# Kernel tuning notes

Hardware: AMD Instinct MI355X
Metric: run time of the kernel (lower is better)

The kernel has to match this reference:

```python
import jax, jax.numpy as jnp
import numpy as np
import math

Q_SHAPES = [(20, 30), (10, 15), (5, 8)]
S_SHAPES = [(20, 30), (10, 15), (5, 8)]
C_IN = 256
C_OUT = 256
NUM_HEADS = 8


def _rel_indices(q_shapes, s_shapes):
    # Faithful translation of QSGA.get_rel_indices: block matrix over pyramid levels.
    rows = []
    for hq, wq in q_shapes:
        cols = []
        for hs, ws in s_shapes:
            ind = np.arange(ws)[None, :] / ws - np.arange(hq)[:, None] / hq  # [hq, ws]
            sc = math.sqrt(ws * hq)
            indx = np.tile(ind, (wq, hs)) * sc                              # [hq*wq, hs*ws]
            indy = np.repeat(np.repeat(ind, wq, axis=0), hs, axis=1) * sc   # [hq*wq, hs*ws]
            indd = indx ** 2 + indy ** 2
            cols.append(np.stack([indd, indx, indy], axis=-1))
        rows.append(np.concatenate(cols, axis=1))
    return jnp.asarray(np.concatenate(rows, axis=0)[None].astype(np.float32))  # [1, Nq, Ns, 3]


def setup_inputs() -> dict:
    key = jax.random.key(0)
    ks = jax.random.split(key, 8)
    B, M = 2, 5
    Nq = sum(h * w for h, w in Q_SHAPES)
    Ns = sum(h * w for h, w in S_SHAPES)
    std = 0.02
    # local_init: v = identity, pos_proj weight zero except col0 = -alphas, gating = ones
    min_a, max_a = 0.002, 0.2
    alphas = np.array([min_a + (max_a - min_a) / NUM_HEADS ** 2.5 * i ** 2.5 for i in range(NUM_HEADS)], np.float32)
    Wp = np.zeros((NUM_HEADS, 3), np.float32)
    Wp[:, 0] = -alphas
    return {
        "q_feat": jax.random.normal(ks[0], (B, Nq, C_IN), jnp.float32),
        "s_feat": jax.random.normal(ks[1], (M, Ns, C_IN), jnp.float32),
        "rel_indices": _rel_indices(Q_SHAPES, S_SHAPES),
        "Wq": jax.random.normal(ks[2], (C_OUT, C_IN), jnp.float32) * std,
        "bq": jnp.zeros((C_OUT,), jnp.float32),
        "Wk": jax.random.normal(ks[3], (C_OUT, C_IN), jnp.float32) * std,
        "bk": jnp.zeros((C_OUT,), jnp.float32),
        "Wv": jnp.eye(C_OUT, C_IN, dtype=jnp.float32),
        "bv": jnp.zeros((C_OUT,), jnp.float32),
        "Wp": jnp.asarray(Wp),
        "bp": jnp.zeros((NUM_HEADS,), jnp.float32),
        "Wo": jax.random.normal(ks[4], (C_OUT, C_OUT), jnp.float32) * std,
        "bo": jnp.zeros((C_OUT,), jnp.float32),
        "gating": jnp.ones((NUM_HEADS,), jnp.float32),
    }


def reference(q_feat, s_feat, rel_indices, Wq, bq, Wk, bk, Wv, bv, Wp, bp, Wo, bo, gating):
    B, Nq, _ = q_feat.shape
    M, Ns, _ = s_feat.shape
    H = gating.shape[0]
    C = Wq.shape[0]
    Dh = C // H
    scale = Dh ** -0.5
    # projections -> [B,H,Nq,Dh], [M,H,Ns,Dh]
    q = (q_feat @ Wq.T + bq).reshape(B, Nq, H, Dh).transpose(0, 2, 1, 3)
    k = (s_feat @ Wk.T + bk).reshape(M, Ns, H, Dh).transpose(0, 2, 1, 3)
    # content scores over all (query image, support image) pairs: [B,M,H,Nq,Ns]
    patch = jnp.einsum('bhqd,mhsd->bmhqs', q, k) * scale
    patch = jax.nn.softmax(patch, axis=-1)
    # positional scores: [1,Nq,Ns,3] -> [1,H,Nq,Ns]
    pos = jax.nn.softmax((rel_indices @ Wp.T + bp).transpose(0, 3, 1, 2), axis=-1)
    g = jax.nn.sigmoid(gating)[None, None, :, None, None]  # [1,1,H,1,1]
    attn = (1.0 - g) * patch + g * pos[:, None]            # broadcast pos over B,M
    attn = attn / attn.sum(axis=-1, keepdims=True)
    v = (s_feat @ Wv.T + bv).reshape(M, Ns, H, Dh).transpose(0, 2, 1, 3)  # [M,H,Ns,Dh]
    out = jnp.einsum('bmhqs,mhsd->bmhqd', attn, v)          # [B,M,H,Nq,Dh]
    out = out.transpose(0, 1, 3, 2, 4).reshape(B, M, Nq, C)  # [B,M,Nq,C]
    return out @ Wo.T + bo
```

## Files before the change

kernel.cpp:

```cpp
#include <hip/hip_runtime.h>
#include <hip/hip_bf16.h>
#include <math.h>

#define B_ 2
#define M_ 5
#define H_ 8
#define C_ 256
#define DH 32
#define NQ 790
#define NS 790
#define QT32 25
#define VROW 800
#define PPAD 800

typedef __attribute__((ext_vector_type(8))) __bf16 bf16x8;
typedef __attribute__((ext_vector_type(16))) float f32x16;
typedef unsigned int u32;
typedef unsigned short u16;

#define LOG2E 1.4426950408889634f

static __device__ __forceinline__ u16 bf16bits(float v) {
  union { __bf16 h; u16 u; } x; x.h = (__bf16)v; return x.u;
}
static __device__ __forceinline__ u32 pack2bf(float a, float b) {
  union { __bf16 h[2]; u32 u; } x; x.h[0] = (__bf16)a; x.h[1] = (__bf16)b; return x.u;
}

#define POS_N 395
#define GEMM0 395
#define PADBLK 544
#define WCVT0 545

#define PROJ_STEP(ACC, BY)                                                 \
  {                                                                        \
    int bcol_ = (BY) * 64 + wc * 32 + lo;                                  \
    const float* wf_ = Wm + (size_t)bcol_ * C_ + k0;                       \
    float4 g0_ = *(const float4*)wf_, g1_ = *(const float4*)(wf_ + 4);     \
    bf16x8 b_;                                                             \
    b_[0]=(__bf16)g0_.x; b_[1]=(__bf16)g0_.y; b_[2]=(__bf16)g0_.z; b_[3]=(__bf16)g0_.w; \
    b_[4]=(__bf16)g1_.x; b_[5]=(__bf16)g1_.y; b_[6]=(__bf16)g1_.z; b_[7]=(__bf16)g1_.w; \
    ACC = __builtin_amdgcn_mfma_f32_32x32x16_bf16(a_, b_, ACC, 0, 0, 0);   \
  }

#define STORE_QK(ACC, BY)                                                  \
  {                                                                        \
    int bcol_ = (BY) * 64 + wc * 32 + lo;                                  \
    float bvv_ = bias[bcol_];                                              \
    _Pragma("unroll")                                                      \
    for (int r_ = 0; r_ < 16; ++r_) {                                      \
      int row_ = (r_ & 3) + 8 * (r_ >> 2) + 4 * hi;                        \
      int grow_ = grow0 + wr * 32 + row_;                                  \
      if (grow_ < R) {                                                     \
        float v_ = (ACC[r_] + bvv_) * scale;                               \
        int seg_ = grow_ / 790, srow_ = grow_ - seg_ * 790;                \
        size_t addr_ = ((size_t)(seg_ * H_ + (bcol_ >> 5)) * 790 + srow_) * 32 + (bcol_ & 31); \
        outp[addr_] = bf16bits(v_);                                        \
      }                                                                    \
    }                                                                      \
  }

#define STORE_V(ACC, BY)                                                   \
  {                                                                        \
    int bcol_ = (BY) * 64 + wc * 32 + lo;                                  \
    float bvv_ = bias[bcol_];                                              \
    int cIn_ = wc * 32 + lo;                                               \
    _Pragma("unroll")                                                      \
    for (int r_ = 0; r_ < 16; ++r_) {                                      \
      int row_ = (r_ & 3) + 8 * (r_ >> 2) + 4 * hi;                        \
      Tls[cIn_][wr * 32 + row_] = bf16bits(ACC[r_] + bvv_);                \
    }                                                                      \
    __syncthreads();                                                       \
    {                                                                      \
      int c_l = tid >> 2, g_l = (tid & 3) * 16;                            \
      int gcol = (BY) * 64 + c_l;                                          \
      int g0v = grow0 + g_l;                                               \
      u16 vals_[16];                                                       \
      _Pragma("unroll")                                                    \
      for (int i_ = 0; i_ < 16; ++i_) vals_[i_] = Tls[c_l][g_l + i_];      \
      int mA_ = g0v / 790, mB_ = (g0v + 15) / 790;                         \
      u16* dst_ = vT2 + (size_t)gcol * (M_ * VROW);                        \
      if (mB_ < M_ && mA_ == mB_) {                                        \
        size_t base_ = (size_t)mA_ * VROW + (g0v - mA_ * 790);             \
        *(uint4*)(dst_ + base_)     = *(uint4*)(vals_);                    \
        *(uint4*)(dst_ + base_ + 8) = *(uint4*)(vals_ + 8);                \
      } else {                                                             \
        _Pragma("unroll")                                                  \
        for (int i_ = 0; i_ < 16; ++i_) {                                  \
          int g_ = g0v + i_;                                               \
          if (g_ < M_ * 790) {                                             \
            int mm_ = g_ / 790, ss_ = g_ - mm_ * 790;                      \
            dst_[(size_t)mm_ * VROW + ss_] = vals_[i_];                    \
          }                                                                \
        }                                                                  \
      }                                                                    \
    }                                                                      \
    __syncthreads();                                                       \
  }

__global__ __launch_bounds__(256) void stage1(const float* __restrict__ qf,
    const float* __restrict__ sf, const float* __restrict__ rel,
    const float* __restrict__ Wq, const float* __restrict__ bq,
    const float* __restrict__ Wk, const float* __restrict__ bk,
    const float* __restrict__ Wv, const float* __restrict__ bv,
    const float* __restrict__ Wp, const float* __restrict__ bp,
    const float* __restrict__ Wo,
    u16* __restrict__ qb, u16* __restrict__ kb, u16* __restrict__ vT2,
    u16* __restrict__ pp, u16* __restrict__ wob, float qscale) {
  __shared__ u16 Tls[64][72];
  int bid = blockIdx.x;
  int tid = threadIdx.x;

  if (bid < POS_N) {
    int wave = tid >> 6, lane = tid & 63;
    int q = bid * 2 + (wave >> 1);
    int h0 = (wave & 1) * 4;
    float rd[13], rx[13], ry[13];
#pragma unroll
    for (int t = 0; t < 13; ++t) {
      int s = lane + 64 * t;
      if (s < NS) {
        const float* rp = rel + ((size_t)q * NS + s) * 3;
        rd[t] = rp[0]; rx[t] = rp[1]; ry[t] = rp[2];
      } else { rd[t] = 0.f; rx[t] = 0.f; ry[t] = 0.f; }
    }
    for (int h = h0; h < h0 + 4; ++h) {
      float w0 = Wp[h * 3] * LOG2E, w1 = Wp[h * 3 + 1] * LOG2E,
            w2 = Wp[h * 3 + 2] * LOG2E, b = bp[h] * LOG2E;
      float lg[13], sm = 0.f;
#pragma unroll
      for (int t = 0; t < 13; ++t) {
        int s = lane + 64 * t;
        float v = rd[t] * w0 + rx[t] * w1 + ry[t] * w2 + b;
        lg[t] = exp2f((s < NS) ? v : -1e30f);
        sm += lg[t];
      }
#pragma unroll
      for (int off = 32; off; off >>= 1) sm += __shfl_xor(sm, off);
      float inv = 1.f / sm;
#pragma unroll
      for (int t = 0; t < 13; ++t) {
        int s = lane + 64 * t;
        if (s < PPAD)
          pp[((size_t)h * NQ + q) * PPAD + s] = (s < NS) ? bf16bits(lg[t] * inv) : (u16)0;
      }
    }
    return;
  }

  if (bid == PADBLK) {
    int c = tid;
#pragma unroll
    for (int m = 0; m < M_; ++m) {
      u32* p = (u32*)(vT2 + (size_t)c * (M_ * VROW) + m * VROW + 790);
#pragma unroll
      for (int i = 0; i < 5; ++i) p[i] = 0;
    }
    return;
  }

  if (bid >= WCVT0) {
    int base = (bid - WCVT0) * 8192;
#pragma unroll
    for (int k = 0; k < 4; ++k) {
      int idx = base + k * 2048 + tid * 8;
      const float* src = Wo + idx;
      float4 f0 = *(const float4*)src, f1 = *(const float4*)(src + 4);
      u16 v[8];
      v[0]=bf16bits(f0.x); v[1]=bf16bits(f0.y); v[2]=bf16bits(f0.z); v[3]=bf16bits(f0.w);
      v[4]=bf16bits(f1.x); v[5]=bf16bits(f1.y); v[6]=bf16bits(f1.z); v[7]=bf16bits(f1.w);
      *(uint4*)(wob + idx) = *(uint4*)v;
    }
    return;
  }

  int j = bid - GEMM0;
  const float* A; const float* Wm; const float* bias; int R; float scale; int role; int bx;
  if (j < 25)      { A = qf; Wm = Wq; bias = bq; R = B_ * NQ; scale = qscale; role = 0; bx = j; }
  else if (j < 87) { A = sf; Wm = Wk; bias = bk; R = M_ * NS; scale = 1.f;    role = 1; bx = j - 25; }
  else             { A = sf; Wm = Wv; bias = bv; R = M_ * NS; scale = 1.f;    role = 2; bx = j - 87; }

  int wave = tid >> 6, lane = tid & 63;
  int lo = lane & 31, hi = lane >> 5;
  int wr = wave >> 1, wc = wave & 1;
  int grow0 = bx * 64;
  int arow = grow0 + wr * 32 + lo;
  int ar = arow < R ? arow : R - 1;

  f32x16 acc0, acc1, acc2, acc3;
#pragma unroll
  for (int r = 0; r < 16; ++r) { acc0[r] = 0.f; acc1[r] = 0.f; acc2[r] = 0.f; acc3[r] = 0.f; }
#pragma unroll
  for (int kk = 0; kk < 16; ++kk) {
    int k0 = kk * 16 + hi * 8;
    const float* af = A + (size_t)ar * C_ + k0;
    float4 f0 = *(const float4*)af, f1 = *(const float4*)(af + 4);
    bf16x8 a_;
    a_[0]=(__bf16)f0.x; a_[1]=(__bf16)f0.y; a_[2]=(__bf16)f0.z; a_[3]=(__bf16)f0.w;
    a_[4]=(__bf16)f1.x; a_[5]=(__bf16)f1.y; a_[6]=(__bf16)f1.z; a_[7]=(__bf16)f1.w;
    PROJ_STEP(acc0, 0);
    PROJ_STEP(acc1, 1);
    PROJ_STEP(acc2, 2);
    PROJ_STEP(acc3, 3);
  }

  if (role < 2) {
    u16* outp = (role == 0) ? qb : kb;
    STORE_QK(acc0, 0);
    STORE_QK(acc1, 1);
    STORE_QK(acc2, 2);
    STORE_QK(acc3, 3);
  } else {
    STORE_V(acc0, 0);
    STORE_V(acc1, 1);
    STORE_V(acc2, 2);
    STORE_V(acc3, 3);
  }
}

static __device__ __forceinline__ void wave_range(int wave, int& st, int& en) {
  st = wave * 6 + (wave ? 1 : 0);
  en = st + (wave ? 6 : 7);
}

#define SM_PV(c_, OACC, ZR, FV0, FV1)                                      \
  {                                                                        \
    float p_[16];                                                          \
    _Pragma("unroll")                                                      \
    for (int r_ = 0; r_ < 16; ++r_) p_[r_] = exp2f(c_[r_]);                \
    float s0_ = p_[0]+p_[1],  s1_ = p_[2]+p_[3];                           \
    float s2_ = p_[4]+p_[5],  s3_ = p_[6]+p_[7];                           \
    float s4_ = p_[8]+p_[9],  s5_ = p_[10]+p_[11];                         \
    float s6_ = p_[12]+p_[13], s7_ = p_[14]+p_[15];                        \
    s0_ += s1_; s2_ += s3_; s4_ += s5_; s6_ += s7_;                        \
    s0_ += s2_; s4_ += s6_;                                                \
    float ts_ = s0_ + s4_;                                                 \
    { float xa_ = ts_, xb_ = ts_;                                          \
      asm("v_permlane32_swap_b32 %0, %1" : "+v"(xa_), "+v"(xb_));          \
      ZR += xa_ + xb_; }                                                   \
    u32 pk_[8];                                                            \
    _Pragma("unroll")                                                      \
    for (int t_ = 0; t_ < 8; ++t_) pk_[t_] = pack2bf(p_[2*t_], p_[2*t_+1]); \
    asm("v_permlane32_swap_b32 %0, %1" : "+v"(pk_[0]), "+v"(pk_[2]));      \
    asm("v_permlane32_swap_b32 %0, %1" : "+v"(pk_[1]), "+v"(pk_[3]));      \
    asm("v_permlane32_swap_b32 %0, %1" : "+v"(pk_[4]), "+v"(pk_[6]));      \
    asm("v_permlane32_swap_b32 %0, %1" : "+v"(pk_[5]), "+v"(pk_[7]));      \
    union { u32 u[4]; bf16x8 v; } pa_, pb_;                                \
    pa_.u[0] = pk_[0]; pa_.u[1] = pk_[1]; pa_.u[2] = pk_[2]; pa_.u[3] = pk_[3]; \
    pb_.u[0] = pk_[4]; pb_.u[1] = pk_[5]; pb_.u[2] = pk_[6]; pb_.u[3] = pk_[7]; \
    OACC = __builtin_amdgcn_mfma_f32_32x32x16_bf16(FV0, pa_.v, OACC, 0, 0, 0); \
    OACC = __builtin_amdgcn_mfma_f32_32x32x16_bf16(FV1, pb_.v, OACC, 0, 0, 0); \
  }

#define TILE_BODY(KC0,KC1, KN0,KN1, IT, NT)                                \
  {                                                                        \
     \
    bf16x8 vf0 = *(const bf16x8*)(vbase + (IT) * 32 + hi8);                \
    bf16x8 vf1 = *(const bf16x8*)(vbase + (IT) * 32 + 16 + hi8);           \
    bf16x8 pf0 = *(const bf16x8*)(pbase + (IT) * 32 + hi8);                \
    bf16x8 pf1 = *(const bf16x8*)(pbase + (IT) * 32 + 16 + hi8);           \
                                             \
    int srn_ = (NT) * 32 + lo; if (srn_ >= NS) srn_ = NS - 1;              \
    KN0 = *(const bf16x8*)(kbase + (size_t)srn_ * 32 + hi8);               \
    KN1 = *(const bf16x8*)(kbase + (size_t)srn_ * 32 + 16 + hi8);          \
    f32x16 c0_ = kZero, c1_ = kZero;                                       \
    c0_ = __builtin_amdgcn_mfma_f32_32x32x16_bf16(KC0, fq00, c0_, 0, 0, 0);\
    c0_ = __builtin_amdgcn_mfma_f32_32x32x16_bf16(KC1, fq01, c0_, 0, 0, 0);\
    c1_ = __builtin_amdgcn_mfma_f32_32x32x16_bf16(KC0, fq10, c1_, 0, 0, 0);\
    c1_ = __builtin_amdgcn_mfma_f32_32x32x16_bf16(KC1, fq11, c1_, 0, 0, 0);\
    Opos = __builtin_amdgcn_mfma_f32_32x32x16_bf16(vf0, pf0, Opos, 0, 0, 0);\
    Opos = __builtin_amdgcn_mfma_f32_32x32x16_bf16(vf1, pf1, Opos, 0, 0, 0);\
    if ((IT) == 24) {                                                      \
      _Pragma("unroll")                                                    \
      for (int r_ = 0; r_ < 16; ++r_) {                                    \
        int sl_ = (r_ & 3) + 8 * (r_ >> 2) + 4 * hi;                       \
        if (768 + sl_ >= NS) { c0_[r_] = -1e30f; c1_[r_] = -1e30f; }       \
      }                                                                    \
    }                                                                      \
    SM_PV(c0_, O0, Z0, vf0, vf1);                                          \
    SM_PV(c1_, O1, Z1, vf0, vf1);                                          \
  }

__global__ __launch_bounds__(256, 3) void attn2(const u16* __restrict__ qb,
    const u16* __restrict__ kb, const u16* __restrict__ vT2,
    const u16* __restrict__ pp, const float* __restrict__ gating,
    u16* __restrict__ opb) {
  int logical = (blockIdx.x & 7) * 125 + (blockIdx.x >> 3);
  int m  = logical % M_;
  int r2 = logical / M_;
  int qt = r2 % QT32;
  int h  = r2 / QT32;
  int tid = threadIdx.x;
  int wave = tid >> 6, lane = tid & 63;
  int lo = lane & 31, hi = lane >> 5, hi8 = hi * 8;
  int qg = qt * 32 + lo;
  int qc = qg < NQ ? qg : NQ - 1;

  const u16* qp0 = qb + ((size_t)(0 * H_ + h) * NQ + qc) * 32 + hi8;
  const u16* qp1 = qb + ((size_t)(1 * H_ + h) * NQ + qc) * 32 + hi8;
  bf16x8 fq00 = *(const bf16x8*)qp0;
  bf16x8 fq01 = *(const bf16x8*)(qp0 + 16);
  bf16x8 fq10 = *(const bf16x8*)qp1;
  bf16x8 fq11 = *(const bf16x8*)(qp1 + 16);
  const u16* kbase = kb + ((size_t)(m * H_ + h) * NS) * 32;
  const u16* vbase = vT2 + (size_t)(h * DH + lo) * (M_ * VROW) + m * VROW;
  const u16* pbase = pp + ((size_t)h * NQ + qc) * PPAD;

  f32x16 O0, O1, Opos, kZero;
#pragma unroll
  for (int r = 0; r < 16; ++r) { O0[r] = 0.f; O1[r] = 0.f; Opos[r] = 0.f; kZero[r] = 0.f; }
  float Z0 = 0.f, Z1 = 0.f;
  int st, en; wave_range(wave, st, en);

  bf16x8 ak0, ak1, bk0, bk1;
  {
    int sr0 = st * 32 + lo; if (sr0 >= NS) sr0 = NS - 1;
    ak0 = *(const bf16x8*)(kbase + (size_t)sr0 * 32 + hi8);
    ak1 = *(const bf16x8*)(kbase + (size_t)sr0 * 32 + 16 + hi8);
  }
  int it = st;
  while (it + 2 <= en) {
    TILE_BODY(ak0, ak1, bk0, bk1, it, it + 1);
    int nt2 = (it + 2 < en) ? it + 2 : it + 1;
    TILE_BODY(bk0, bk1, ak0, ak1, it + 1, nt2);
    it += 2;
  }
  if (it < en) TILE_BODY(ak0, ak1, bk0, bk1, it, it);

  __shared__ float Os[4][32][33];
  __shared__ float Zs[4][32];
  float g = 1.f / (1.f + __expf(-gating[h]));
  int d = tid & 31, qi = tid >> 5;
  float oc0[4], oc1[4];

#pragma unroll
  for (int r = 0; r < 16; ++r) {
    int dd = (r & 3) + 8 * (r >> 2) + 4 * hi;
    Os[wave][dd][lo] = O0[r];
  }
  if (hi == 0) Zs[wave][lo] = Z0;
  __syncthreads();
#pragma unroll
  for (int k = 0; k < 4; ++k) {
    int ql = qi + 8 * k;
    float zg = Zs[0][ql] + Zs[1][ql] + Zs[2][ql] + Zs[3][ql];
    float oc = Os[0][d][ql] + Os[1][d][ql] + Os[2][d][ql] + Os[3][d][ql];
    oc0[k] = (1.f - g) * oc / zg;
  }
  __syncthreads();

#pragma unroll
  for (int r = 0; r < 16; ++r) {
    int dd = (r & 3) + 8 * (r >> 2) + 4 * hi;
    Os[wave][dd][lo] = O1[r];
  }
  if (hi == 0) Zs[wave][lo] = Z1;
  __syncthreads();
#pragma unroll
  for (int k = 0; k < 4; ++k) {
    int ql = qi + 8 * k;
    float zg = Zs[0][ql] + Zs[1][ql] + Zs[2][ql] + Zs[3][ql];
    float oc = Os[0][d][ql] + Os[1][d][ql] + Os[2][d][ql] + Os[3][d][ql];
    oc1[k] = (1.f - g) * oc / zg;
  }
  __syncthreads();

#pragma unroll
  for (int r = 0; r < 16; ++r) {
    int dd = (r & 3) + 8 * (r >> 2) + 4 * hi;
    Os[wave][dd][lo] = Opos[r];
  }
  __syncthreads();
  u16* out0 = opb + ((size_t)(0 * M_ + m) * NQ) * C_ + h * DH + d;
  u16* out1 = opb + ((size_t)(1 * M_ + m) * NQ) * C_ + h * DH + d;
#pragma unroll
  for (int k = 0; k < 4; ++k) {
    int ql = qi + 8 * k;
    int qgl = qt * 32 + ql;
    if (qgl < NQ) {
      float op = Os[0][d][ql] + Os[1][d][ql] + Os[2][d][ql] + Os[3][d][ql];
      out0[(size_t)qgl * C_] = bf16bits(oc0[k] + g * op);
      out1[(size_t)qgl * C_] = bf16bits(oc1[k] + g * op);
    }
  }
}

__global__ __launch_bounds__(256) void out_gemm(const u16* __restrict__ Ap,
    const u16* __restrict__ Wb, const float* __restrict__ bias,
    float* __restrict__ outp, int R) {
  int tid = threadIdx.x;
  int wave = tid >> 6, lane = tid & 63;
  int lo = lane & 31, hi = lane >> 5;
  int wr = wave >> 1, wc = wave & 1;
  int arow = blockIdx.x * 64 + wr * 32 + lo;
  int ar = arow < R ? arow : R - 1;
  int bcolA = blockIdx.y * 128 + wc * 32 + lo;
  int bcolB = bcolA + 64;
  f32x16 accA, accB;
#pragma unroll
  for (int r = 0; r < 16; ++r) { accA[r] = 0.f; accB[r] = 0.f; }
#pragma unroll
  for (int kk = 0; kk < 16; ++kk) {
    int k0 = kk * 16 + hi * 8;
    bf16x8 a = *(const bf16x8*)(Ap + (size_t)ar * C_ + k0);
    bf16x8 bA = *(const bf16x8*)(Wb + (size_t)bcolA * C_ + k0);
    bf16x8 bB = *(const bf16x8*)(Wb + (size_t)bcolB * C_ + k0);
    accA = __builtin_amdgcn_mfma_f32_32x32x16_bf16(a, bA, accA, 0, 0, 0);
    accB = __builtin_amdgcn_mfma_f32_32x32x16_bf16(a, bB, accB, 0, 0, 0);
  }
  float bvA = bias[bcolA], bvB = bias[bcolB];
#pragma unroll
  for (int r = 0; r < 16; ++r) {
    int row = (r & 3) + 8 * (r >> 2) + 4 * hi;
    int grow = blockIdx.x * 64 + wr * 32 + row;
    if (grow < R) {
      outp[(size_t)grow * C_ + bcolA] = accA[r] + bvA;
      outp[(size_t)grow * C_ + bcolB] = accB[r] + bvB;
    }
  }
}

extern "C" void kernel_launch(void* const* d_in, const int* in_sizes, int n_in,
                              void* d_out, int out_size, void* d_ws, size_t ws_size,
                              hipStream_t stream) {
  const float* q_feat = (const float*)d_in[0];
  const float* s_feat = (const float*)d_in[1];
  const float* rel    = (const float*)d_in[2];
  const float* Wq = (const float*)d_in[3];
  const float* bq = (const float*)d_in[4];
  const float* Wk = (const float*)d_in[5];
  const float* bk = (const float*)d_in[6];
  const float* Wv = (const float*)d_in[7];
  const float* bv = (const float*)d_in[8];
  const float* Wp = (const float*)d_in[9];
  const float* bp = (const float*)d_in[10];
  const float* Wo = (const float*)d_in[11];
  const float* bo = (const float*)d_in[12];
  const float* gating = (const float*)d_in[13];
  float* out = (float*)d_out;

  char* w = (char*)d_ws;
  u16* qb  = (u16*)w;
  u16* kb  = (u16*)(w + 808960);
  u16* vT2 = (u16*)(w + 2831360);
  u16* pp  = (u16*)(w + 4879360);
  u16* opb = (u16*)(w + 14991360);
  u16* wob = (u16*)(w + 19036160);

  const float QSCALE = 0.17677669529663687f * 1.4426950408889634f;

  stage1<<<553, 256, 0, stream>>>(q_feat, s_feat, rel, Wq, bq, Wk, bk, Wv, bv,
                                  Wp, bp, Wo, qb, kb, vT2, pp, wob, QSCALE);
  attn2<<<1000, 256, 0, stream>>>(qb, kb, vT2, pp, gating, opb);
  out_gemm<<<dim3(124, 2), 256, 0, stream>>>(opb, wob, bo, out, B_ * M_ * NQ);
}
```

Before: 69.90 us.

## Process two query tiles per attention block to reuse K/V fragment loads

Each attention block now handles a pair of 32-row query tiles (A and B), so every K and V fragment loaded per key tile feeds twice as many MFMAs. The grid shrinks from 1000 to 520 blocks and launch bounds drop to 2 blocks per CU to make room for the doubled accumulators. Inline-asm permlane swaps are also replaced with the compiler builtin, which may let the compiler schedule them better. The cost is higher register pressure, lower occupancy, one extra padded tile of wasted work (13 pairs for 25 tiles), and a longer serialized epilogue with more barriers.

```diff
diff --git a/kernel.cpp b/kernel.cpp
--- a/kernel.cpp
+++ b/kernel.cpp
@@ -10,11 +10,13 @@
 #define NQ 790
 #define NS 790
 #define QT32 25
+#define QTP 13
 #define VROW 800
 #define PPAD 800
 
 typedef __attribute__((ext_vector_type(8))) __bf16 bf16x8;
 typedef __attribute__((ext_vector_type(16))) float f32x16;
+typedef __attribute__((ext_vector_type(2))) unsigned int u32x2;
 typedef unsigned int u32;
 typedef unsigned short u16;
 
@@ -25,6 +27,16 @@
 }
 static __device__ __forceinline__ u32 pack2bf(float a, float b) {
   union { __bf16 h[2]; u32 u; } x; x.h[0] = (__bf16)a; x.h[1] = (__bf16)b; return x.u;
+}
+static __device__ __forceinline__ float halfswap_sum(float ts) {
+  union { float f; u32 u; } c; c.f = ts;
+  u32x2 r = __builtin_amdgcn_permlane32_swap(c.u, c.u, false, false);
+  union { u32 u; float f; } a, b; a.u = r[0]; b.u = r[1];
+  return a.f + b.f;
+}
+static __device__ __forceinline__ void pswap(u32& x, u32& y) {
+  u32x2 r = __builtin_amdgcn_permlane32_swap(x, y, false, false);
+  x = r[0]; y = r[1];
 }
 
 #define POS_N 395
@@ -234,17 +246,14 @@
     float s6_ = p_[12]+p_[13], s7_ = p_[14]+p_[15];                        \
     s0_ += s1_; s2_ += s3_; s4_ += s5_; s6_ += s7_;                        \
     s0_ += s2_; s4_ += s6_;                                                \
-    float ts_ = s0_ + s4_;                                                 \
-    { float xa_ = ts_, xb_ = ts_;                                          \
-      asm("v_permlane32_swap_b32 %0, %1" : "+v"(xa_), "+v"(xb_));          \
-      ZR += xa_ + xb_; }                                                   \
+    ZR += halfswap_sum(s0_ + s4_);                                         \
     u32 pk_[8];                                                            \
     _Pragma("unroll")                                                      \
     for (int t_ = 0; t_ < 8; ++t_) pk_[t_] = pack2bf(p_[2*t_], p_[2*t_+1]); \
-    asm("v_permlane32_swap_b32 %0, %1" : "+v"(pk_[0]), "+v"(pk_[2]));      \
-    asm("v_permlane32_swap_b32 %0, %1" : "+v"(pk_[1]), "+v"(pk_[3]));      \
-    asm("v_permlane32_swap_b32 %0, %1" : "+v"(pk_[4]), "+v"(pk_[6]));      \
-    asm("v_permlane32_swap_b32 %0, %1" : "+v"(pk_[5]), "+v"(pk_[7]));      \
+    pswap(pk_[0], pk_[2]);                                                 \
+    pswap(pk_[1], pk_[3]);                                                 \
+    pswap(pk_[4], pk_[6]);                                                 \
+    pswap(pk_[5], pk_[7]);                                                 \
     union { u32 u[4]; bf16x8 v; } pa_, pb_;                                \
     pa_.u[0] = pk_[0]; pa_.u[1] = pk_[1]; pa_.u[2] = pk_[2]; pa_.u[3] = pk_[3]; \
     pb_.u[0] = pk_[4]; pb_.u[1] = pk_[5]; pb_.u[2] = pk_[6]; pb_.u[3] = pk_[7]; \
@@ -252,64 +261,90 @@
     OACC = __builtin_amdgcn_mfma_f32_32x32x16_bf16(FV1, pb_.v, OACC, 0, 0, 0); \
   }
 
+#define MASK_TAIL(c_)                                                      \
+    { _Pragma("unroll")                                                    \
+      for (int r_ = 0; r_ < 16; ++r_) {                                    \
+        int sl_ = (r_ & 3) + 8 * (r_ >> 2) + 4 * hi;                       \
+        if (768 + sl_ >= NS) c_[r_] = -1e30f;                              \
+      } }
+
 #define TILE_BODY(KC0,KC1, KN0,KN1, IT, NT)                                \
   {                                                                        \
-     \
     bf16x8 vf0 = *(const bf16x8*)(vbase + (IT) * 32 + hi8);                \
     bf16x8 vf1 = *(const bf16x8*)(vbase + (IT) * 32 + 16 + hi8);           \
-    bf16x8 pf0 = *(const bf16x8*)(pbase + (IT) * 32 + hi8);                \
-    bf16x8 pf1 = *(const bf16x8*)(pbase + (IT) * 32 + 16 + hi8);           \
-                                             \
+    bf16x8 pA0 = *(const bf16x8*)(pbA + (IT) * 32 + hi8);                  \
+    bf16x8 pA1 = *(const bf16x8*)(pbA + (IT) * 32 + 16 + hi8);             \
+    bf16x8 pB0 = *(const bf16x8*)(pbB + (IT) * 32 + hi8);                  \
+    bf16x8 pB1 = *(const bf16x8*)(pbB + (IT) * 32 + 16 + hi8);             \
     int srn_ = (NT) * 32 + lo; if (srn_ >= NS) srn_ = NS - 1;              \
     KN0 = *(const bf16x8*)(kbase + (size_t)srn_ * 32 + hi8);               \
     KN1 = *(const bf16x8*)(kbase + (size_t)srn_ * 32 + 16 + hi8);          \
-    f32x16 c0_ = kZero, c1_ = kZero;                                       \
-    c0_ = __builtin_amdgcn_mfma_f32_32x32x16_bf16(KC0, fq00, c0_, 0, 0, 0);\
-    c0_ = __builtin_amdgcn_mfma_f32_32x32x16_bf16(KC1, fq01, c0_, 0, 0, 0);\
-    c1_ = __builtin_amdgcn_mfma_f32_32x32x16_bf16(KC0, fq10, c1_, 0, 0, 0);\
-    c1_ = __builtin_amdgcn_mfma_f32_32x32x16_bf16(KC1, fq11, c1_, 0, 0, 0);\
-    Opos = __builtin_amdgcn_mfma_f32_32x32x16_bf16(vf0, pf0, Opos, 0, 0, 0);\
-    Opos = __builtin_amdgcn_mfma_f32_32x32x16_bf16(vf1, pf1, Opos, 0, 0, 0);\
-    if ((IT) == 24) {                                                      \
-      _Pragma("unroll")                                                    \
-      for (int r_ = 0; r_ < 16; ++r_) {                                    \
-        int sl_ = (r_ & 3) + 8 * (r_ >> 2) + 4 * hi;                       \
-        if (768 + sl_ >= NS) { c0_[r_] = -1e30f; c1_[r_] = -1e30f; }       \
-      }                                                                    \
-    }                                                                      \
-    SM_PV(c0_, O0, Z0, vf0, vf1);                                          \
-    SM_PV(c1_, O1, Z1, vf0, vf1);                                          \
-  }
-
-__global__ __launch_bounds__(256, 3) void attn2(const u16* __restrict__ qb,
+    OposA = __builtin_amdgcn_mfma_f32_32x32x16_bf16(vf0, pA0, OposA, 0, 0, 0); \
+    OposA = __builtin_amdgcn_mfma_f32_32x32x16_bf16(vf1, pA1, OposA, 0, 0, 0); \
+    OposB = __builtin_amdgcn_mfma_f32_32x32x16_bf16(vf0, pB0, OposB, 0, 0, 0); \
+    OposB = __builtin_amdgcn_mfma_f32_32x32x16_bf16(vf1, pB1, OposB, 0, 0, 0); \
+    {                                                                      \
+      f32x16 c0_ = kZero, c1_ = kZero;                                     \
+      c0_ = __builtin_amdgcn_mfma_f32_32x32x16_bf16(KC0, fqA00, c0_, 0, 0, 0); \
+      c0_ = __builtin_amdgcn_mfma_f32_32x32x16_bf16(KC1, fqA01, c0_, 0, 0, 0); \
+      c1_ = __builtin_amdgcn_mfma_f32_32x32x16_bf16(KC0, fqA10, c1_, 0, 0, 0); \
+      c1_ = __builtin_amdgcn_mfma_f32_32x32x16_bf16(KC1, fqA11, c1_, 0, 0, 0); \
+      if ((IT) == 24) { MASK_TAIL(c0_); MASK_TAIL(c1_); }                  \
+      SM_PV(c0_, OA0, ZA0, vf0, vf1);                                      \
+      SM_PV(c1_, OA1, ZA1, vf0, vf1);                                      \
+    }                                                                      \
+    {                                                                      \
+      f32x16 c0_ = kZero, c1_ = kZero;                                     \
+      c0_ = __builtin_amdgcn_mfma_f32_32x32x16_bf16(KC0, fqB00, c0_, 0, 0, 0); \
+      c0_ = __builtin_amdgcn_mfma_f32_32x32x16_bf16(KC1, fqB01, c0_, 0, 0, 0); \
+      c1_ = __builtin_amdgcn_mfma_f32_32x32x16_bf16(KC0, fqB10, c1_, 0, 0, 0); \
+      c1_ = __builtin_amdgcn_mfma_f32_32x32x16_bf16(KC1, fqB11, c1_, 0, 0, 0); \
+      if ((IT) == 24) { MASK_TAIL(c0_); MASK_TAIL(c1_); }                  \
+      SM_PV(c0_, OB0, ZB0, vf0, vf1);                                      \
+      SM_PV(c1_, OB1, ZB1, vf0, vf1);                                      \
+    }                                                                      \
+  }
+
+__global__ __launch_bounds__(256, 2) void attn2(const u16* __restrict__ qb,
     const u16* __restrict__ kb, const u16* __restrict__ vT2,
     const u16* __restrict__ pp, const float* __restrict__ gating,
     u16* __restrict__ opb) {
-  int logical = (blockIdx.x & 7) * 125 + (blockIdx.x >> 3);
-  int m  = logical % M_;
-  int r2 = logical / M_;
-  int qt = r2 % QT32;
-  int h  = r2 / QT32;
+  int logical = (blockIdx.x & 7) * 65 + (blockIdx.x >> 3);
+  int m   = logical % M_;
+  int r2  = logical / M_;
+  int qtp = r2 % QTP;
+  int h   = r2 / QTP;
+  int qtA = qtp * 2, qtB = qtp * 2 + 1;
   int tid = threadIdx.x;
   int wave = tid >> 6, lane = tid & 63;
   int lo = lane & 31, hi = lane >> 5, hi8 = hi * 8;
-  int qg = qt * 32 + lo;
-  int qc = qg < NQ ? qg : NQ - 1;
-
-  const u16* qp0 = qb + ((size_t)(0 * H_ + h) * NQ + qc) * 32 + hi8;
-  const u16* qp1 = qb + ((size_t)(1 * H_ + h) * NQ + qc) * 32 + hi8;
-  bf16x8 fq00 = *(const bf16x8*)qp0;
-  bf16x8 fq01 = *(const bf16x8*)(qp0 + 16);
-  bf16x8 fq10 = *(const bf16x8*)qp1;
-  bf16x8 fq11 = *(const bf16x8*)(qp1 + 16);
+  int qgA = qtA * 32 + lo;  int qcA = qgA < NQ ? qgA : NQ - 1;
+  int qgB = qtB * 32 + lo;  int qcB = qgB < NQ ? qgB : NQ - 1;
+
+  const u16* qpA0 = qb + ((size_t)(0 * H_ + h) * NQ + qcA) * 32 + hi8;
+  const u16* qpA1 = qb + ((size_t)(1 * H_ + h) * NQ + qcA) * 32 + hi8;
+  const u16* qpB0 = qb + ((size_t)(0 * H_ + h) * NQ + qcB) * 32 + hi8;
+  const u16* qpB1 = qb + ((size_t)(1 * H_ + h) * NQ + qcB) * 32 + hi8;
+  bf16x8 fqA00 = *(const bf16x8*)qpA0;
+  bf16x8 fqA01 = *(const bf16x8*)(qpA0 + 16);
+  bf16x8 fqA10 = *(const bf16x8*)qpA1;
+  bf16x8 fqA11 = *(const bf16x8*)(qpA1 + 16);
+  bf16x8 fqB00 = *(const bf16x8*)qpB0;
+  bf16x8 fqB01 = *(const bf16x8*)(qpB0 + 16);
+  bf16x8 fqB10 = *(const bf16x8*)qpB1;
+  bf16x8 fqB11 = *(const bf16x8*)(qpB1 + 16);
   const u16* kbase = kb + ((size_t)(m * H_ + h) * NS) * 32;
   const u16* vbase = vT2 + (size_t)(h * DH + lo) * (M_ * VROW) + m * VROW;
-  const u16* pbase = pp + ((size_t)h * NQ + qc) * PPAD;
-
-  f32x16 O0, O1, Opos, kZero;
-#pragma unroll
-  for (int r = 0; r < 16; ++r) { O0[r] = 0.f; O1[r] = 0.f; Opos[r] = 0.f; kZero[r] = 0.f; }
-  float Z0 = 0.f, Z1 = 0.f;
+  const u16* pbA = pp + ((size_t)h * NQ + qcA) * PPAD;
+  const u16* pbB = pp + ((size_t)h * NQ + qcB) * PPAD;
+
+  f32x16 OA0, OA1, OB0, OB1, OposA, OposB, kZero;
+#pragma unroll
+  for (int r = 0; r < 16; ++r) {
+    OA0[r] = 0.f; OA1[r] = 0.f; OB0[r] = 0.f; OB1[r] = 0.f;
+    OposA[r] = 0.f; OposB[r] = 0.f; kZero[r] = 0.f;
+  }
+  float ZA0 = 0.f, ZA1 = 0.f, ZB0 = 0.f, ZB1 = 0.f;
   int st, en; wave_range(wave, st, en);
 
   bf16x8 ak0, ak1, bk0, bk1;
@@ -331,58 +366,64 @@
   __shared__ float Zs[4][32];
   float g = 1.f / (1.f + __expf(-gating[h]));
   int d = tid & 31, qi = tid >> 5;
-  float oc0[4], oc1[4];
-
-#pragma unroll
-  for (int r = 0; r < 16; ++r) {
-    int dd = (r & 3) + 8 * (r >> 2) + 4 * hi;
-    Os[wave][dd][lo] = O0[r];
-  }
-  if (hi == 0) Zs[wave][lo] = Z0;
-  __syncthreads();
-#pragma unroll
-  for (int k = 0; k < 4; ++k) {
-    int ql = qi + 8 * k;
-    float zg = Zs[0][ql] + Zs[1][ql] + Zs[2][ql] + Zs[3][ql];
-    float oc = Os[0][d][ql] + Os[1][d][ql] + Os[2][d][ql] + Os[3][d][ql];
-    oc0[k] = (1.f - g) * oc / zg;
-  }
-  __syncthreads();
-
-#pragma unroll
-  for (int r = 0; r < 16; ++r) {
-    int dd = (r & 3) + 8 * (r >> 2) + 4 * hi;
-    Os[wave][dd][lo] = O1[r];
-  }
-  if (hi == 0) Zs[wave][lo] = Z1;
-  __syncthreads();
-#pragma unroll
-  for (int k = 0; k < 4; ++k) {
-    int ql = qi + 8 * k;
-    float zg = Zs[0][ql] + Zs[1][ql] + Zs[2][ql] + Zs[3][ql];
-    float oc = Os[0][d][ql] + Os[1][d][ql] + Os[2][d][ql] + Os[3][d][ql];
-    oc1[k] = (1.f - g) * oc / zg;
-  }
-  __syncthreads();
-
-#pragma unroll
-  for (int r = 0; r < 16; ++r) {
-    int dd = (r & 3) + 8 * (r >> 2) + 4 * hi;
-    Os[wave][dd][lo] = Opos[r];
-  }
-  __syncthreads();
-  u16* out0 = opb + ((size_t)(0 * M_ + m) * NQ) * C_ + h * DH + d;
-  u16* out1 = opb + ((size_t)(1 * M_ + m) * NQ) * C_ + h * DH + d;
-#pragma unroll
-  for (int k = 0; k < 4; ++k) {
-    int ql = qi + 8 * k;
-    int qgl = qt * 32 + ql;
-    if (qgl < NQ) {
-      float op = Os[0][d][ql] + Os[1][d][ql] + Os[2][d][ql] + Os[3][d][ql];
-      out0[(size_t)qgl * C_] = bf16bits(oc0[k] + g * op);
-      out1[(size_t)qgl * C_] = bf16bits(oc1[k] + g * op);
-    }
-  }
+
+#define MERGE_QT(OX0, OX1, OPOSX, ZX0, ZX1, QT)                            \
+  {                                                                        \
+    float oc0[4], oc1[4];                                                  \
+    _Pragma("unroll")                                                      \
+    for (int r = 0; r < 16; ++r) {                                         \
+      int dd = (r & 3) + 8 * (r >> 2) + 4 * hi;                            \
+      Os[wave][dd][lo] = OX0[r];                                           \
+    }                                                                      \
+    if (hi == 0) Zs[wave][lo] = ZX0;                                       \
+    __syncthreads();                                                       \
+    _Pragma("unroll")                                                      \
+    for (int k = 0; k < 4; ++k) {                                          \
+      int ql = qi + 8 * k;                                                 \
+      float zg = Zs[0][ql] + Zs[1][ql] + Zs[2][ql] + Zs[3][ql];            \
+      float oc = Os[0][d][ql] + Os[1][d][ql] + Os[2][d][ql] + Os[3][d][ql];\
+      oc0[k] = (1.f - g) * oc / zg;                                        \
+    }                                                                      \
+    __syncthreads();                                                       \
+    _Pragma("unroll")                                                      \
+    for (int r = 0; r < 16; ++r) {                                         \
+      int dd = (r & 3) + 8 * (r >> 2) + 4 * hi;                            \
+      Os[wave][dd][lo] = OX1[r];                                           \
+    }                                                                      \
+    if (hi == 0) Zs[wave][lo] = ZX1;                                       \
+    __syncthreads();                                                       \
+    _Pragma("unroll")                                                      \
+    for (int k = 0; k < 4; ++k) {                                          \
+      int ql = qi + 8 * k;                                                 \
+      float zg = Zs[0][ql] + Zs[1][ql] + Zs[2][ql] + Zs[3][ql];            \
+      float oc = Os[0][d][ql] + Os[1][d][ql] + Os[2][d][ql] + Os[3][d][ql];\
+      oc1[k] = (1.f - g) * oc / zg;                                        \
+    }                                                                      \
+    __syncthreads();                                                       \
+    _Pragma("unroll")                                                      \
+    for (int r = 0; r < 16; ++r) {                                         \
+      int dd = (r & 3) + 8 * (r >> 2) + 4 * hi;                            \
+      Os[wave][dd][lo] = OPOSX[r];                                         \
+    }                                                                      \
+    __syncthreads();                                                       \
+    u16* out0 = opb + ((size_t)(0 * M_ + m) * NQ) * C_ + h * DH + d;       \
+    u16* out1 = opb + ((size_t)(1 * M_ + m) * NQ) * C_ + h * DH + d;       \
+    _Pragma("unroll")                                                      \
+    for (int k = 0; k < 4; ++k) {                                          \
+      int ql = qi + 8 * k;                                                 \
+      int qgl = (QT) * 32 + ql;                                            \
+      if (qgl < NQ) {                                                      \
+        float op = Os[0][d][ql] + Os[1][d][ql] + Os[2][d][ql] + Os[3][d][ql]; \
+        out0[(size_t)qgl * C_] = bf16bits(oc0[k] + g * op);                \
+        out1[(size_t)qgl * C_] = bf16bits(oc1[k] + g * op);                \
+      }                                                                    \
+    }                                                                      \
+    __syncthreads();                                                       \
+  }
+
+  MERGE_QT(OA0, OA1, OposA, ZA0, ZA1, qtA);
+  MERGE_QT(OB0, OB1, OposB, ZB0, ZB1, qtB);
+#undef MERGE_QT
 }
 
 __global__ __launch_bounds__(256) void out_gemm(const u16* __restrict__ Ap,
@@ -451,6 +492,6 @@
 
   stage1<<<553, 256, 0, stream>>>(q_feat, s_feat, rel, Wq, bq, Wk, bk, Wv, bv,
                                   Wp, bp, Wo, qb, kb, vT2, pp, wob, QSCALE);
-  attn2<<<1000, 256, 0, stream>>>(qb, kb, vT2, pp, gating, opb);
+  attn2<<<520, 256, 0, stream>>>(qb, kb, vT2, pp, gating, opb);
   out_gemm<<<dim3(124, 2), 256, 0, stream>>>(opb, wob, bo, out, B_ * M_ * NQ);
 }
```

Result: slower. 82.65 us (+18.2%).
